# Kernel tuning notes

Measured on AMD Instinct MI355X. Metric: run time of the kernel, lower is better.

Reference implementation:

```python
import jax, jax.numpy as jnp
import numpy as np

DIM = 2048
NUM_HEADS = 16
HEAD_DIM = 128
SEQ_LEN = 2048
BATCH = 2


def _rope_tables(seq_len, head_dim, dtype):
    inv_freq = 1.0 / (10000.0 ** (np.arange(0, head_dim, 2, dtype=np.float32) / head_dim))
    t = np.arange(seq_len, dtype=np.float32)
    freqs = np.outer(t, inv_freq)                      # [S, D/2]
    emb = np.concatenate([freqs, freqs], axis=-1)      # [S, D]
    return jnp.asarray(np.cos(emb), dtype=dtype), jnp.asarray(np.sin(emb), dtype=dtype)


def _rotate_half(x):
    x1, x2 = jnp.split(x, 2, axis=-1)
    return jnp.concatenate([-x2, x1], axis=-1)


def setup_inputs() -> dict:
    key = jax.random.key(0)
    k1, k2, k3 = jax.random.split(key, 3)
    x = jax.random.normal(k1, (BATCH, SEQ_LEN, DIM), dtype=jnp.float32)
    # xavier_uniform-like scale for linear weights [out, in]
    lim_qkv = float(np.sqrt(6.0 / (3 * DIM + DIM)))
    lim_out = float(np.sqrt(6.0 / (DIM + DIM)))
    qkv_w = jax.random.uniform(k2, (3 * NUM_HEADS * HEAD_DIM, DIM), jnp.float32, -lim_qkv, lim_qkv)
    out_w = jax.random.uniform(k3, (DIM, DIM), jnp.float32, -lim_out, lim_out)
    return {"x": x, "qkv_w": qkv_w, "out_w": out_w}


def reference(x, qkv_w, out_w):
    B, S, _ = x.shape
    H, D = NUM_HEADS, HEAD_DIM
    qkv = jnp.einsum('bsd,ed->bse', x, qkv_w)                 # [B,S,3*H*D]
    qkv = qkv.reshape(B, S, 3, H, D)
    q = jnp.transpose(qkv[:, :, 0], (0, 2, 1, 3))             # [B,H,S,D]
    k = jnp.transpose(qkv[:, :, 1], (0, 2, 1, 3))
    v = jnp.transpose(qkv[:, :, 2], (0, 2, 1, 3))
    cos, sin = _rope_tables(S, D, x.dtype)                    # [S,D]
    q = q * cos + _rotate_half(q) * sin
    k = k * cos + _rotate_half(k) * sin
    scale = 1.0 / jnp.sqrt(jnp.asarray(D, x.dtype))
    scores = jnp.einsum('bhqd,bhkd->bhqk', q, k) * scale       # [B,H,S,S]
    neg = jnp.finfo(x.dtype).min
    causal = jnp.triu(jnp.ones((S, S), dtype=bool), k=1)
    scores = jnp.where(causal[None, None], scores + neg, scores)
    attn = jax.nn.softmax(scores, axis=-1)
    out = jnp.einsum('bhqk,bhkd->bhqd', attn, v)               # [B,H,S,D]
    out = jnp.transpose(out, (0, 2, 1, 3)).reshape(B, S, H * D)
    return jnp.einsum('bsd,ed->bse', out, out_w)
```

## Files before the change

kernel.cpp:

```cpp
#include <hip/hip_runtime.h>
#include <math.h>

#define DIMN   2048
#define NHEADS 16
#define HDIM   128
#define SEQ    2048
#define BATCH  2
#define SCALE  0.08838834764831845f
#define BHSD   (BATCH*NHEADS*SEQ*HDIM)

typedef unsigned short u16;
typedef __attribute__((ext_vector_type(8))) unsigned short ushort8v;
typedef __attribute__((ext_vector_type(8))) short bf16x8;
typedef __attribute__((ext_vector_type(4))) float f32x4;

#define MFMA16(a,b,c) __builtin_amdgcn_mfma_f32_16x16x32_bf16(a,b,c,0,0,0)

__device__ inline float bf2f(u16 h) {
    union { unsigned u; float f; } v; v.u = ((unsigned)h) << 16; return v.f;
}
__device__ inline u16 f2bf(float f) {
    union { float f; unsigned u; } v; v.f = f;
    unsigned r = v.u + 0x7FFF + ((v.u >> 16) & 1);
    return (u16)(r >> 16);
}
__device__ inline ushort8v pack8(const float4& a, const float4& b) {
    ushort8v r;
    r[0]=f2bf(a.x); r[1]=f2bf(a.y); r[2]=f2bf(a.z); r[3]=f2bf(a.w);
    r[4]=f2bf(b.x); r[5]=f2bf(b.y); r[6]=f2bf(b.z); r[7]=f2bf(b.w);
    return r;
}

__global__ __launch_bounds__(64) void rope_table_kernel(float* __restrict__ cosT,
                                                        float* __restrict__ sinT) {
    int pos = blockIdx.x;
    int i   = threadIdx.x;
    double e    = (double)(2 * i) / 128.0;
    float  invf = (float)pow(10000.0, -e);
    float  freq = (float)pos * invf;
    double fr = (double)freq;
    cosT[pos*64 + i] = (float)cos(fr);
    sinT[pos*64 + i] = (float)sin(fr);
}

template<int MODE>
__global__ __launch_bounds__(256) void gemm_mfma(const void* __restrict__ Av,
                                                 const float* __restrict__ W,
                                                 void* __restrict__ o0,
                                                 void* __restrict__ o1,
                                                 void* __restrict__ o2,
                                                 int K) {
    __shared__ __align__(16) u16 Alds[128][40];
    __shared__ __align__(16) u16 Blds[128][40];

    const int tid  = threadIdx.x;
    const int srow = tid >> 1;
    const int skk  = (tid & 1) * 16;
    const int w    = tid >> 6;
    const int l    = tid & 63;
    const int lr   = l & 15;
    const int lk   = l >> 4;
    const int wr   = (w >> 1) * 64;
    const int wc   = (w & 1) * 64;
    const int bx   = blockIdx.x;
    const int by   = blockIdx.y;

    const float* aF = (const float*)Av + (long)(by*128 + srow) * K;
    const u16*   aH = (const u16*)Av   + (long)(by*128 + srow) * K;
    const float* bF = W + (long)(bx*128 + srow) * K;

    f32x4 acc[4][4];
    #pragma unroll
    for (int i = 0; i < 4; ++i)
        #pragma unroll
        for (int j = 0; j < 4; ++j) acc[i][j] = f32x4{0.f,0.f,0.f,0.f};

    float4 av[4]; ushort8v ah[2]; float4 bv[4];
    if constexpr (MODE == 0) {
        #pragma unroll
        for (int j = 0; j < 4; ++j) av[j] = *(const float4*)(aF + skk + 4*j);
    } else {
        #pragma unroll
        for (int j = 0; j < 2; ++j) ah[j] = *(const ushort8v*)(aH + skk + 8*j);
    }
    #pragma unroll
    for (int j = 0; j < 4; ++j) bv[j] = *(const float4*)(bF + skk + 4*j);

    for (int k0 = 0; k0 < K; k0 += 32) {
        __syncthreads();
        if constexpr (MODE == 0) {
            *(ushort8v*)&Alds[srow][skk]     = pack8(av[0], av[1]);
            *(ushort8v*)&Alds[srow][skk + 8] = pack8(av[2], av[3]);
        } else {
            *(ushort8v*)&Alds[srow][skk]     = ah[0];
            *(ushort8v*)&Alds[srow][skk + 8] = ah[1];
        }
        *(ushort8v*)&Blds[srow][skk]     = pack8(bv[0], bv[1]);
        *(ushort8v*)&Blds[srow][skk + 8] = pack8(bv[2], bv[3]);
        __syncthreads();

        if (k0 + 32 < K) {
            if constexpr (MODE == 0) {
                #pragma unroll
                for (int j = 0; j < 4; ++j) av[j] = *(const float4*)(aF + k0+32 + skk + 4*j);
            } else {
                #pragma unroll
                for (int j = 0; j < 2; ++j) ah[j] = *(const ushort8v*)(aH + k0+32 + skk + 8*j);
            }
            #pragma unroll
            for (int j = 0; j < 4; ++j) bv[j] = *(const float4*)(bF + k0+32 + skk + 4*j);
        }

        bf16x8 af[4], bf[4];
        #pragma unroll
        for (int mr = 0; mr < 4; ++mr)
            af[mr] = *(const bf16x8*)&Alds[wr + mr*16 + lr][lk*8];
        #pragma unroll
        for (int nr = 0; nr < 4; ++nr)
            bf[nr] = *(const bf16x8*)&Blds[wc + nr*16 + lr][lk*8];
        #pragma unroll
        for (int mr = 0; mr < 4; ++mr)
            #pragma unroll
            for (int nr = 0; nr < 4; ++nr)
                acc[mr][nr] = MFMA16(af[mr], bf[nr], acc[mr][nr]);
    }

    if constexpr (MODE == 0) {
        const int t = bx >> 4;
        const int h = bx & 15;
        u16* dst = (t == 0) ? (u16*)o0 : (t == 1) ? (u16*)o1 : (u16*)o2;
        #pragma unroll
        for (int mr = 0; mr < 4; ++mr)
            #pragma unroll
            for (int r = 0; r < 4; ++r) {
                int m = by*128 + wr + mr*16 + lk*4 + r;
                int b = m >> 11, s = m & 2047;
                long ro = ((long)(b*NHEADS + h) * SEQ + s) * HDIM;
                #pragma unroll
                for (int nr = 0; nr < 4; ++nr)
                    dst[ro + wc + nr*16 + lr] = f2bf(acc[mr][nr][r]);
            }
    } else {
        float* out = (float*)o0;
        #pragma unroll
        for (int mr = 0; mr < 4; ++mr)
            #pragma unroll
            for (int r = 0; r < 4; ++r) {
                long m = by*128 + wr + mr*16 + lk*4 + r;
                #pragma unroll
                for (int nr = 0; nr < 4; ++nr)
                    out[m*DIMN + bx*128 + wc + nr*16 + lr] = acc[mr][nr][r];
            }
    }
}

__global__ __launch_bounds__(256) void rope_apply_kernel(u16* __restrict__ q,
                                                         u16* __restrict__ k,
                                                         const float* __restrict__ cosT,
                                                         const float* __restrict__ sinT) {
    int idx = blockIdx.x * 256 + threadIdx.x;
    int i  = idx & 63;
    int s  = (idx >> 6) & (SEQ - 1);
    int bh = idx >> 17;
    long base = ((long)bh * SEQ + s) * HDIM;
    float c  = cosT[s*64 + i];
    float sn = sinT[s*64 + i];
    float q1 = bf2f(q[base + i]), q2 = bf2f(q[base + 64 + i]);
    q[base + i]      = f2bf(q1 * c - q2 * sn);
    q[base + 64 + i] = f2bf(q2 * c + q1 * sn);
    float k1 = bf2f(k[base + i]), k2 = bf2f(k[base + 64 + i]);
    k[base + i]      = f2bf(k1 * c - k2 * sn);
    k[base + 64 + i] = f2bf(k2 * c + k1 * sn);
}

__global__ __launch_bounds__(256) void attn_mfma(const u16* __restrict__ qb,
                                                 const u16* __restrict__ kb,
                                                 const u16* __restrict__ vb,
                                                 u16* __restrict__ ao) {
    __shared__ __align__(16) u16 Klds[32][136];
    __shared__ __align__(16) u16 Vt[128][40];
    __shared__ __align__(16) u16 Pst[64][40];

    const int tid = threadIdx.x;
    const int w   = tid >> 6;
    const int l   = tid & 63;
    const int lr  = l & 15;
    const int lk  = l >> 4;
    const int bq  = (SEQ/64 - 1) - blockIdx.x;
    const int h   = blockIdx.y;
    const int b   = blockIdx.z;
    const int q0  = bq * 64;

    const long headoff = ((long)(b*NHEADS + h)) * SEQ * HDIM;
    const u16* qh = qb + headoff;
    const u16* kh = kb + headoff;
    const u16* vh = vb + headoff;

    bf16x8 qf[4];
    {
        const u16* qrow = qh + (long)(q0 + w*16 + lr) * HDIM;
        #pragma unroll
        for (int ds = 0; ds < 4; ++ds)
            qf[ds] = *(const bf16x8*)(qrow + ds*32 + lk*8);
    }

    f32x4 accO[8];
    #pragma unroll
    for (int nb = 0; nb < 8; ++nb) accO[nb] = f32x4{0.f,0.f,0.f,0.f};
    float m_[4], l_[4];
    #pragma unroll
    for (int r = 0; r < 4; ++r) { m_[r] = -1e30f; l_[r] = 0.f; }

    const int srow = tid >> 3;
    const int sd   = (tid & 7) * 16;

    const int ntiles = 2*bq + 2;
    for (int t = 0; t < ntiles; ++t) {
        const int kt0 = t * 32;
        __syncthreads();

        {
            const u16* ksrc = kh + (long)(kt0 + srow) * HDIM + sd;
            ushort8v k0v = *(const ushort8v*)ksrc;
            ushort8v k1v = *(const ushort8v*)(ksrc + 8);
            *(ushort8v*)&Klds[srow][sd]     = k0v;
            *(ushort8v*)&Klds[srow][sd + 8] = k1v;
            const u16* vsrc = vh + (long)(kt0 + srow) * HDIM + sd;
            ushort8v v0 = *(const ushort8v*)vsrc;
            ushort8v v1 = *(const ushort8v*)(vsrc + 8);
            #pragma unroll
            for (int e = 0; e < 8; ++e) Vt[sd + e][srow]     = v0[e];
            #pragma unroll
            for (int e = 0; e < 8; ++e) Vt[sd + 8 + e][srow] = v1[e];
        }
        __syncthreads();

        f32x4 sv[2];
        #pragma unroll
        for (int kbk = 0; kbk < 2; ++kbk) {
            sv[kbk] = f32x4{0.f,0.f,0.f,0.f};
            #pragma unroll
            for (int ds = 0; ds < 4; ++ds) {
                bf16x8 kf = *(const bf16x8*)&Klds[kbk*16 + lr][ds*32 + lk*8];
                sv[kbk] = MFMA16(qf[ds], kf, sv[kbk]);
            }
        }

        const bool masked = (t >= 2*bq);
        #pragma unroll
        for (int kbk = 0; kbk < 2; ++kbk)
            #pragma unroll
            for (int r = 0; r < 4; ++r) {
                float v = sv[kbk][r] * SCALE;
                if (masked) {
                    int kg = kt0 + kbk*16 + lr;
                    int rg = q0 + w*16 + lk*4 + r;
                    if (kg > rg) v = -1e30f;
                }
                sv[kbk][r] = v;
            }

        #pragma unroll
        for (int r = 0; r < 4; ++r) {
            float mx = fmaxf(sv[0][r], sv[1][r]);
            #pragma unroll
            for (int o = 1; o < 16; o <<= 1) mx = fmaxf(mx, __shfl_xor(mx, o, 64));
            float mn = fmaxf(m_[r], mx);
            float ef = expf(m_[r] - mn);
            float p0 = expf(sv[0][r] - mn);
            float p1 = expf(sv[1][r] - mn);
            float rs = p0 + p1;
            #pragma unroll
            for (int o = 1; o < 16; o <<= 1) rs += __shfl_xor(rs, o, 64);
            l_[r] = l_[r] * ef + rs;
            m_[r] = mn;
            #pragma unroll
            for (int nb = 0; nb < 8; ++nb) accO[nb][r] *= ef;
            int qrow = w*16 + lk*4 + r;
            Pst[qrow][lr]      = f2bf(p0);
            Pst[qrow][16 + lr] = f2bf(p1);
        }
        __syncthreads();

        bf16x8 pf = *(const bf16x8*)&Pst[w*16 + lr][lk*8];
        #pragma unroll
        for (int nb = 0; nb < 8; ++nb) {
            bf16x8 vf = *(const bf16x8*)&Vt[nb*16 + lr][lk*8];
            accO[nb] = MFMA16(pf, vf, accO[nb]);
        }
    }

    #pragma unroll
    for (int r = 0; r < 4; ++r) {
        float inv = 1.0f / l_[r];
        long ro = ((long)b * SEQ + q0 + w*16 + lk*4 + r) * DIMN + h * HDIM;
        #pragma unroll
        for (int nb = 0; nb < 8; ++nb)
            ao[ro + nb*16 + lr] = f2bf(accO[nb][r] * inv);
    }
}

extern "C" void kernel_launch(void* const* d_in, const int* in_sizes, int n_in,
                              void* d_out, int out_size, void* d_ws, size_t ws_size,
                              hipStream_t stream) {
    const float* x     = (const float*)d_in[0];
    const float* qkv_w = (const float*)d_in[1];
    const float* out_w = (const float*)d_in[2];
    float* out = (float*)d_out;
    float* ws  = (float*)d_ws;

    float* cosT = ws;
    float* sinT = ws + SEQ*64;
    u16* qb = (u16*)(ws + 2*SEQ*64);
    u16* kb = qb + BHSD;
    u16* vb = kb + BHSD;
    u16* ao = vb + BHSD;

    rope_table_kernel<<<dim3(SEQ), dim3(64), 0, stream>>>(cosT, sinT);

    gemm_mfma<0><<<dim3(48, 32), dim3(256), 0, stream>>>(x, qkv_w, qb, kb, vb, DIMN);

    rope_apply_kernel<<<dim3((BATCH*NHEADS*SEQ*64)/256), dim3(256), 0, stream>>>(qb, kb, cosT, sinT);

    attn_mfma<<<dim3(SEQ/64, NHEADS, BATCH), dim3(256), 0, stream>>>(qb, kb, vb, ao);

    gemm_mfma<1><<<dim3(16, 32), dim3(256), 0, stream>>>(ao, out_w, out, nullptr, nullptr, DIMN);
}
```

Before: 759.7 us.

## Write V transposed from QKV GEMM and load K/V fragments directly from global

The QKV GEMM epilogue now writes V in a per-head transposed [D][S] layout using 4-wide stores. The attention kernel drops its K and V shared-memory staging, including the scalar transpose into LDS, and reads MFMA fragments for K and V straight from global memory. This removes LDS traffic and one barrier per tile. The cost is that each wave re-reads K/V from global or cache with less coalesced access patterns.

```diff
diff --git a/kernel.cpp b/kernel.cpp
--- a/kernel.cpp
+++ b/kernel.cpp
@@ -128,18 +128,36 @@
     if constexpr (MODE == 0) {
         const int t = bx >> 4;
         const int h = bx & 15;
-        u16* dst = (t == 0) ? (u16*)o0 : (t == 1) ? (u16*)o1 : (u16*)o2;
-        #pragma unroll
-        for (int mr = 0; mr < 4; ++mr)
-            #pragma unroll
-            for (int r = 0; r < 4; ++r) {
-                int m = by*128 + wr + mr*16 + lk*4 + r;
-                int b = m >> 11, s = m & 2047;
-                long ro = ((long)(b*NHEADS + h) * SEQ + s) * HDIM;
-                #pragma unroll
-                for (int nr = 0; nr < 4; ++nr)
-                    dst[ro + wc + nr*16 + lr] = f2bf(acc[mr][nr][r]);
-            }
+        if (t < 2) {
+            u16* dst = (t == 0) ? (u16*)o0 : (u16*)o1;
+            #pragma unroll
+            for (int mr = 0; mr < 4; ++mr)
+                #pragma unroll
+                for (int r = 0; r < 4; ++r) {
+                    int m = by*128 + wr + mr*16 + lk*4 + r;
+                    int b = m >> 11, s = m & 2047;
+                    long ro = ((long)(b*NHEADS + h) * SEQ + s) * HDIM;
+                    #pragma unroll
+                    for (int nr = 0; nr < 4; ++nr)
+                        dst[ro + wc + nr*16 + lr] = f2bf(acc[mr][nr][r]);
+                }
+        } else {
+            u16* dst = (u16*)o2;
+            #pragma unroll
+            for (int mr = 0; mr < 4; ++mr) {
+                int m0 = by*128 + wr + mr*16 + lk*4;
+                int b0 = m0 >> 11, s0 = m0 & 2047;
+                long hb = (long)(b0*NHEADS + h) * SEQ * HDIM;
+                #pragma unroll
+                for (int nr = 0; nr < 4; ++nr) {
+                    long ad = hb + (long)(wc + nr*16 + lr) * SEQ + s0;
+                    ushort4 vv;
+                    vv.x = f2bf(acc[mr][nr][0]); vv.y = f2bf(acc[mr][nr][1]);
+                    vv.z = f2bf(acc[mr][nr][2]); vv.w = f2bf(acc[mr][nr][3]);
+                    *(ushort4*)&dst[ad] = vv;
+                }
+            }
+        }
     } else {
         float* out = (float*)o0;
         #pragma unroll
@@ -175,10 +193,8 @@
 
 __global__ __launch_bounds__(256) void attn_mfma(const u16* __restrict__ qb,
                                                  const u16* __restrict__ kb,
-                                                 const u16* __restrict__ vb,
+                                                 const u16* __restrict__ vt,
                                                  u16* __restrict__ ao) {
-    __shared__ __align__(16) u16 Klds[32][136];
-    __shared__ __align__(16) u16 Vt[128][40];
     __shared__ __align__(16) u16 Pst[64][40];
 
     const int tid = threadIdx.x;
@@ -194,7 +210,7 @@
     const long headoff = ((long)(b*NHEADS + h)) * SEQ * HDIM;
     const u16* qh = qb + headoff;
     const u16* kh = kb + headoff;
-    const u16* vh = vb + headoff;
+    const u16* vh = vt + headoff;
 
     bf16x8 qf[4];
     {
@@ -211,40 +227,26 @@
     #pragma unroll
     for (int r = 0; r < 4; ++r) { m_[r] = -1e30f; l_[r] = 0.f; }
 
-    const int srow = tid >> 3;
-    const int sd   = (tid & 7) * 16;
-
     const int ntiles = 2*bq + 2;
     for (int t = 0; t < ntiles; ++t) {
         const int kt0 = t * 32;
-        __syncthreads();
-
-        {
-            const u16* ksrc = kh + (long)(kt0 + srow) * HDIM + sd;
-            ushort8v k0v = *(const ushort8v*)ksrc;
-            ushort8v k1v = *(const ushort8v*)(ksrc + 8);
-            *(ushort8v*)&Klds[srow][sd]     = k0v;
-            *(ushort8v*)&Klds[srow][sd + 8] = k1v;
-            const u16* vsrc = vh + (long)(kt0 + srow) * HDIM + sd;
-            ushort8v v0 = *(const ushort8v*)vsrc;
-            ushort8v v1 = *(const ushort8v*)(vsrc + 8);
-            #pragma unroll
-            for (int e = 0; e < 8; ++e) Vt[sd + e][srow]     = v0[e];
-            #pragma unroll
-            for (int e = 0; e < 8; ++e) Vt[sd + 8 + e][srow] = v1[e];
-        }
-        __syncthreads();
 
         f32x4 sv[2];
         #pragma unroll
         for (int kbk = 0; kbk < 2; ++kbk) {
             sv[kbk] = f32x4{0.f,0.f,0.f,0.f};
+            const u16* krow = kh + (long)(kt0 + kbk*16 + lr) * HDIM;
             #pragma unroll
             for (int ds = 0; ds < 4; ++ds) {
-                bf16x8 kf = *(const bf16x8*)&Klds[kbk*16 + lr][ds*32 + lk*8];
+                bf16x8 kf = *(const bf16x8*)(krow + ds*32 + lk*8);
                 sv[kbk] = MFMA16(qf[ds], kf, sv[kbk]);
             }
         }
+
+        bf16x8 vf[8];
+        #pragma unroll
+        for (int nb = 0; nb < 8; ++nb)
+            vf[nb] = *(const bf16x8*)(vh + (long)(nb*16 + lr) * SEQ + kt0 + lk*8);
 
         const bool masked = (t >= 2*bq);
         #pragma unroll
@@ -260,6 +262,7 @@
                 sv[kbk][r] = v;
             }
 
+        float p0[4], p1[4];
         #pragma unroll
         for (int r = 0; r < 4; ++r) {
             float mx = fmaxf(sv[0][r], sv[1][r]);
@@ -267,27 +270,30 @@
             for (int o = 1; o < 16; o <<= 1) mx = fmaxf(mx, __shfl_xor(mx, o, 64));
             float mn = fmaxf(m_[r], mx);
             float ef = expf(m_[r] - mn);
-            float p0 = expf(sv[0][r] - mn);
-            float p1 = expf(sv[1][r] - mn);
-            float rs = p0 + p1;
+            p0[r] = expf(sv[0][r] - mn);
+            p1[r] = expf(sv[1][r] - mn);
+            float rs = p0[r] + p1[r];
             #pragma unroll
             for (int o = 1; o < 16; o <<= 1) rs += __shfl_xor(rs, o, 64);
             l_[r] = l_[r] * ef + rs;
             m_[r] = mn;
             #pragma unroll
             for (int nb = 0; nb < 8; ++nb) accO[nb][r] *= ef;
+        }
+
+        __syncthreads();
+        #pragma unroll
+        for (int r = 0; r < 4; ++r) {
             int qrow = w*16 + lk*4 + r;
-            Pst[qrow][lr]      = f2bf(p0);
-            Pst[qrow][16 + lr] = f2bf(p1);
+            Pst[qrow][lr]      = f2bf(p0[r]);
+            Pst[qrow][16 + lr] = f2bf(p1[r]);
         }
         __syncthreads();
 
         bf16x8 pf = *(const bf16x8*)&Pst[w*16 + lr][lk*8];
         #pragma unroll
-        for (int nb = 0; nb < 8; ++nb) {
-            bf16x8 vf = *(const bf16x8*)&Vt[nb*16 + lr][lk*8];
-            accO[nb] = MFMA16(pf, vf, accO[nb]);
-        }
+        for (int nb = 0; nb < 8; ++nb)
+            accO[nb] = MFMA16(pf, vf[nb], accO[nb]);
     }
 
     #pragma unroll
@@ -313,16 +319,16 @@
     float* sinT = ws + SEQ*64;
     u16* qb = (u16*)(ws + 2*SEQ*64);
     u16* kb = qb + BHSD;
-    u16* vb = kb + BHSD;
-    u16* ao = vb + BHSD;
+    u16* vt = kb + BHSD;
+    u16* ao = vt + BHSD;
 
     rope_table_kernel<<<dim3(SEQ), dim3(64), 0, stream>>>(cosT, sinT);
 
-    gemm_mfma<0><<<dim3(48, 32), dim3(256), 0, stream>>>(x, qkv_w, qb, kb, vb, DIMN);
+    gemm_mfma<0><<<dim3(48, 32), dim3(256), 0, stream>>>(x, qkv_w, qb, kb, vt, DIMN);
 
     rope_apply_kernel<<<dim3((BATCH*NHEADS*SEQ*64)/256), dim3(256), 0, stream>>>(qb, kb, cosT, sinT);
 
-    attn_mfma<<<dim3(SEQ/64, NHEADS, BATCH), dim3(256), 0, stream>>>(qb, kb, vb, ao);
+    attn_mfma<<<dim3(SEQ/64, NHEADS, BATCH), dim3(256), 0, stream>>>(qb, kb, vt, ao);
 
     gemm_mfma<1><<<dim3(16, 32), dim3(256), 0, stream>>>(ao, out_w, out, nullptr, nullptr, DIMN);
 }
```

Measured after the change: 984.9 us. 1.3x slower.
